# Kernel tuning notes

Measured on AMD Instinct MI355X. Metric: run time of the kernel, lower is better.

Reference implementation:

```python
import jax, jax.numpy as jnp
import numpy as np
from jax import lax

NUM_CLASSES = 9
N_BOXES = 6
LEVELS = [(32, 256), (16, 128), (8, 64), (4, 32), (2, 16), (1, 8)]
BATCH = 8


def _conv(x, w, b):
    # x: [N,C,H,W], w: [O,I,3,3] -> same-padded stride-1 conv (padding=1)
    y = lax.conv_general_dilated(x, w, window_strides=(1, 1), padding='SAME',
                                 dimension_numbers=('NCHW', 'OIHW', 'NCHW'))
    return y + b[None, :, None, None]


def _head(x, ws, bs, w_out, b_out):
    for i in range(4):
        x = jax.nn.relu(_conv(x, ws[i], bs[i]))
    return _conv(x, w_out, b_out)


def setup_inputs() -> dict:
    key = jax.random.key(0)
    ks = jax.random.split(key, 12)
    inp = {}
    for i, (h, w) in enumerate(LEVELS):
        inp[f'feat{i}'] = jax.random.normal(ks[i], (BATCH, 256, h, w), dtype=jnp.float32)
    std = 0.01  # matches _init_improved_weights: normal(0, 0.01), bias=0
    inp['reg_w'] = jax.random.normal(ks[6], (4, 256, 256, 3, 3), dtype=jnp.float32) * std
    inp['reg_b'] = jnp.zeros((4, 256), dtype=jnp.float32)
    inp['reg_w_out'] = jax.random.normal(ks[7], (N_BOXES * 4, 256, 3, 3), dtype=jnp.float32) * std
    inp['reg_b_out'] = jnp.zeros((N_BOXES * 4,), dtype=jnp.float32)
    inp['cls_w'] = jax.random.normal(ks[8], (4, 256, 256, 3, 3), dtype=jnp.float32) * std
    inp['cls_b'] = jnp.zeros((4, 256), dtype=jnp.float32)
    inp['cls_w_out'] = jax.random.normal(ks[9], (N_BOXES * NUM_CLASSES, 256, 3, 3), dtype=jnp.float32) * std
    inp['cls_b_out'] = jnp.zeros((N_BOXES * NUM_CLASSES,), dtype=jnp.float32)
    return inp


def reference(feat0, feat1, feat2, feat3, feat4, feat5,
              reg_w, reg_b, reg_w_out, reg_b_out,
              cls_w, cls_b, cls_w_out, cls_b_out):
    features = [feat0, feat1, feat2, feat3, feat4, feat5]
    locations, confidences = [], []
    for x in features:
        n = x.shape[0]
        bbox_delta = _head(x, reg_w, reg_b, reg_w_out, reg_b_out).reshape(n, 4, -1)
        bbox_conf = _head(x, cls_w, cls_b, cls_w_out, cls_b_out).reshape(n, NUM_CLASSES, -1)
        locations.append(bbox_delta)
        confidences.append(bbox_conf)
    bbox_delta = jnp.concatenate(locations, axis=2)   # [N, 4, total_anchors]
    confs = jnp.concatenate(confidences, axis=2)      # [N, num_classes, total_anchors]
    return (bbox_delta, confs)
```

## Files before the change

### kernel.cpp

```cpp
#include <hip/hip_runtime.h>
#include <hip/hip_bf16.h>


typedef float  f32x4 __attribute__((ext_vector_type(4)));
typedef int    i32x4 __attribute__((ext_vector_type(4)));
typedef int    i32x2 __attribute__((ext_vector_type(2)));
typedef __bf16 bfrag __attribute__((ext_vector_type(8)));
typedef __bf16 bf4   __attribute__((ext_vector_type(4)));

struct LevelD {
  int H, W, logW, logHW, P, HW, act_off, aoff, blk_start, pos_start;
};
struct Desc  { LevelD lv[6]; };
struct FPtrs { const float* f[6]; };

#define ACT_ELEMS  24735744
#define WREG_OFF   0
#define WCLS_OFF   2359296
#define WREGO_OFF  4718592
#define WCLSO_OFF  4773888
#define ACT0_OFF   4898304
#define ACT1_OFF   29634048
#define ACT2_OFF   54369792
#define WS_ELEMS   54369792ull
#define TOTAL_ANCH 65520
#define CLS_BASE   2096640
#define NPAD_JOBS  9264

__device__ __forceinline__ void glds16(const __bf16* g, __bf16* l) {
  __builtin_amdgcn_global_load_lds(
      (const __attribute__((address_space(1))) void*)g,
      (__attribute__((address_space(3))) void*)l, 16, 0, 0);
}

__device__ __forceinline__ int xcd_swz(int b, int nwg) {
  int xcd = b & 7;
  int q = nwg >> 3, r = nwg & 7;
  int base = (xcd < r) ? xcd * (q + 1) : r * (q + 1) + (xcd - r) * q;
  return base + (b >> 3);
}

__global__ __launch_bounds__(256) void padzero_k(__bf16* __restrict__ act, int nbuf)
{
  static const int kHh[6]   = {32, 16, 8, 4, 2, 1};
  static const int kWw[6]   = {256, 128, 64, 32, 16, 8};
  static const int kOff[6]  = {0, 17965056, 22757376, 24109056, 24526848, 24674304};
  static const int kPer[6]  = {580, 292, 148, 76, 40, 22};
  static const int kCum[7]  = {0, 4640, 6976, 8160, 8768, 9088, 9264};
  int job  = blockIdx.x * 4 + (threadIdx.x >> 6);
  int lane = threadIdx.x & 63;
  int nb = job / NPAD_JOBS;
  if (nb >= nbuf) return;
  int e8 = job - nb * NPAD_JOBS;
  int li = 0;
  #pragma unroll
  for (int i = 1; i < 6; ++i) li = (e8 >= kCum[i]) ? i : li;
  int r = e8 - kCum[li];
  int per = kPer[li];
  int n = r / per;
  int e = r - n * per;
  int H = kHh[li], W = kWw[li], Wp = W + 2;
  int y, x;
  if (e < 2 * Wp) {
    y = (e < Wp) ? 0 : (H + 1);
    x = (e < Wp) ? e : (e - Wp);
  } else {
    int e2 = e - 2 * Wp;
    x = (e2 < H) ? 0 : (W + 1);
    y = 1 + ((e2 < H) ? e2 : (e2 - H));
  }
  size_t base = (size_t)nb * ACT_ELEMS + kOff[li]
              + ((size_t)((n * (H + 2) + y) * Wp + x) << 8) + (lane << 2);
  i32x2 z = {0, 0};
  *(i32x2*)(act + base) = z;
}

__global__ __launch_bounds__(256) void prep_k(const float* __restrict__ w,
                                              __bf16* __restrict__ o, int total)
{
  for (int i = blockIdx.x * 256 + threadIdx.x; i < total; i += gridDim.x * 256) {
    int co = i / 2304;
    int r  = i - co * 2304;
    int t  = r >> 8;
    int ci = r & 255;
    o[i] = (__bf16)w[((co << 8) + ci) * 9 + t];
  }
}

__global__ __launch_bounds__(256) void convert_k(FPtrs fp, __bf16* __restrict__ act, Desc d)
{
  __shared__ __bf16 T[16 * 264];
  int b  = blockIdx.x;
  int p0 = b << 4;
  int li = 0;
  #pragma unroll
  for (int i = 1; i < 6; ++i) li = (p0 >= d.lv[i].pos_start) ? i : li;
  LevelD L = d.lv[li];
  int lp  = b * 16 - L.pos_start;
  int tid = threadIdx.x;
  int pl = tid & 15;
  int p  = lp + pl;
  int n  = p >> L.logHW;
  int y  = (p >> L.logW) & (L.H - 1);
  int x  = p & (L.W - 1);
  const float* src = fp.f[li];
  size_t base = (size_t)n * ((size_t)L.HW << 8) + (size_t)y * L.W + x;
  int c0 = tid >> 4;
  #pragma unroll
  for (int it = 0; it < 16; ++it) {
    int c = c0 + (it << 4);
    T[pl * 264 + c] = (__bf16)src[base + (size_t)c * L.HW];
  }
  __syncthreads();
  int p2 = tid >> 4;
  int cc = (tid & 15) << 4;
  int pg = lp + p2;
  int n2 = pg >> L.logHW;
  int y2 = (pg >> L.logW) & (L.H - 1);
  int x2 = pg & (L.W - 1);
  __bf16* dst = act + L.act_off +
      ((size_t)((n2 * (L.H + 2) + y2 + 1) * (L.W + 2) + x2 + 1) << 8) + cc;
  i32x4 v0 = *(const i32x4*)&T[p2 * 264 + cc];
  i32x4 v1 = *(const i32x4*)&T[p2 * 264 + cc + 8];
  *(i32x4*)dst       = v0;
  *(i32x4*)(dst + 8) = v1;
}

__global__ __launch_bounds__(512, 4)
void conv_mid_k(const __bf16* __restrict__ inb, __bf16* __restrict__ outb,
                const __bf16* __restrict__ wT, const float* __restrict__ bias,
                Desc d)
{
  __shared__ __bf16 Al[2][256 * 32];
  __shared__ __bf16 Bl[2][96 * 32];
  int b  = xcd_swz(blockIdx.x, 912);
  int li = 0;
  #pragma unroll
  for (int i = 1; i < 6; ++i) li = (b >= d.lv[i].blk_start) ? i : li;
  LevelD L = d.lv[li];
  int p0 = (b - L.blk_start) * 96;
  int tid  = threadIdx.x;
  int lane = tid & 63;
  int wv   = tid >> 6;
  int wm = wv >> 1, wn = wv & 1;
  int fr = lane & 15, fg = lane >> 4;
  int Wp = L.W + 2;

  int rsub = lane >> 2;
  int slot = lane & 3;
  int sw   = slot ^ ((rsub >> 1) & 3);

  const __bf16* gA[2];
  int ldsA[2];
  #pragma unroll
  for (int r = 0; r < 2; ++r) {
    int row = (r << 7) + (wv << 4) + rsub;
    gA[r] = wT + row * 2304 + (sw << 3);
    ldsA[r] = ((r << 7) + (wv << 4)) << 5;
  }
  const __bf16* gB;
  int ldsB;
  {
    int row = (wv << 4) + rsub;
    int p  = p0 + row;
    int pc = (p < L.P) ? p : 0;
    int n  = pc >> L.logHW;
    int y  = (pc >> L.logW) & (L.H - 1);
    int x  = pc & (L.W - 1);
    gB = inb + L.act_off + (((n * (L.H + 2) + y) * Wp + x) << 8) + (sw << 3);
    ldsB = (wv << 4) << 5;
  }

  int csw = ((fg ^ ((fr >> 1) & 3)) << 3);
  int offA[4], offB[3];
  #pragma unroll
  for (int mf = 0; mf < 4; ++mf)
    offA[mf] = (((wm << 6) + (mf << 4) + fr) << 5) + csw;
  #pragma unroll
  for (int nf = 0; nf < 3; ++nf)
    offB[nf] = ((wn * 48 + (nf << 4) + fr) << 5) + csw;

  auto stage = [&](int k, int bb) {
    int t  = k >> 3;
    int c0 = (k & 7) << 5;
    int ky = (t >= 6) ? 2 : (t >= 3 ? 1 : 0);
    int kx = t - ky * 3;
    int koffA = (t << 8) + c0;
    int koffB = ((ky * Wp + kx) << 8) + c0;
    glds16(gA[0] + koffA, &Al[bb][ldsA[0]]);
    glds16(gA[1] + koffA, &Al[bb][ldsA[1]]);
    if (wv < 6) glds16(gB + koffB, &Bl[bb][ldsB]);
  };

  f32x4 acc[4][3] = {};

  stage(0, 0);
  #pragma unroll 1
  for (int k = 0; k < 72; ++k) {
    int cur = k & 1;
    __syncthreads();
    if (k < 71) stage(k + 1, cur ^ 1);
    bfrag af[4], bfv[3];
    #pragma unroll
    for (int mf = 0; mf < 4; ++mf) af[mf]  = *(const bfrag*)&Al[cur][offA[mf]];
    #pragma unroll
    for (int nf = 0; nf < 3; ++nf) bfv[nf] = *(const bfrag*)&Bl[cur][offB[nf]];
    #pragma unroll
    for (int mf = 0; mf < 4; ++mf)
      #pragma unroll
      for (int nf = 0; nf < 3; ++nf)
        acc[mf][nf] = __builtin_amdgcn_mfma_f32_16x16x32_bf16(af[mf], bfv[nf],
                                                              acc[mf][nf], 0, 0, 0);
  }

  #pragma unroll
  for (int nf = 0; nf < 3; ++nf) {
    int pp = p0 + wn * 48 + (nf << 4) + fr;
    if (pp >= L.P) continue;
    int n2 = pp >> L.logHW;
    int y2 = (pp >> L.logW) & (L.H - 1);
    int x2 = pp & (L.W - 1);
    __bf16* ob = outb + L.act_off + (((n2 * (L.H + 2) + y2 + 1) * Wp + x2 + 1) << 8);
    #pragma unroll
    for (int mf = 0; mf < 4; ++mf) {
      int cob = (wm << 6) + (mf << 4) + (fg << 2);
      f32x4 bb = *(const f32x4*)(bias + cob);
      f32x4 v  = acc[mf][nf];
      bf4 ov;
      #pragma unroll
      for (int j = 0; j < 4; ++j) ov[j] = (__bf16)fmaxf(v[j] + bb[j], 0.0f);
      *(bf4*)(ob + cob) = ov;
    }
  }
}

__global__ __launch_bounds__(256, 3)
void conv_out_k(const __bf16* __restrict__ inb, const __bf16* __restrict__ wT,
                const float* __restrict__ biasO, float* __restrict__ dout,
                Desc d, int Cout, int isCls)
{
  __shared__ __bf16 Asm[2][64 * 32];
  __shared__ __bf16 Bsm[2][128 * 32];
  int b  = xcd_swz(blockIdx.x, 683);
  int li = 0;
  #pragma unroll
  for (int i = 1; i < 6; ++i) li = (b >= d.lv[i].blk_start) ? i : li;
  LevelD L = d.lv[li];
  int p0 = (b - L.blk_start) << 7;
  int tid  = threadIdx.x;
  int lane = tid & 63;
  int wv   = tid >> 6;
  int fr = lane & 15, fg = lane >> 4;
  int Wp = L.W + 2;
  int nmf = (Cout + 15) >> 4;

  int rsub = lane >> 2;
  int slot = lane & 3;
  int sw   = slot ^ ((rsub >> 1) & 3);

  const __bf16* gA0;
  {
    int row = (wv << 4) + rsub;
    int co  = (row < Cout) ? row : 0;
    gA0 = wT + co * 2304 + (sw << 3);
  }
  const __bf16* gB[2];
  #pragma unroll
  for (int j = 0; j < 2; ++j) {
    int row = (j << 6) + (wv << 4) + rsub;
    int p  = p0 + row;
    int pc = (p < L.P) ? p : 0;
    int n = pc >> L.logHW, y = (pc >> L.logW) & (L.H - 1), x = pc & (L.W - 1);
    gB[j] = inb + L.act_off + (((n * (L.H + 2) + y) * Wp + x) << 8) + (sw << 3);
  }
  int dW = (wv << 4) << 5;

  int csw = ((fg ^ ((fr >> 1) & 3)) << 3);
  int offA[4], offB[2];
  #pragma unroll
  for (int mf = 0; mf < 4; ++mf)
    offA[mf] = (((mf << 4) + fr) << 5) + csw;
  #pragma unroll
  for (int nf = 0; nf < 2; ++nf)
    offB[nf] = (((wv << 5) + (nf << 4) + fr) << 5) + csw;

  auto stage = [&](int k, int bb) {
    int t  = k >> 3;
    int ky = (t >= 6) ? 2 : (t >= 3 ? 1 : 0);
    int kx = t - ky * 3;
    int ka = (t << 8) + ((k & 7) << 5);
    int kb = ((ky * Wp + kx) << 8) + ((k & 7) << 5);
    glds16(gA0 + ka, &Asm[bb][dW]);
    glds16(gB[0] + kb, &Bsm[bb][dW]);
    glds16(gB[1] + kb, &Bsm[bb][2048 + dW]);
  };

  f32x4 acc[4][2] = {};

  stage(0, 0);
  #pragma unroll 1
  for (int k = 0; k < 72; ++k) {
    int cur = k & 1;
    __syncthreads();
    if (k < 71) stage(k + 1, cur ^ 1);
    bfrag af[4], bfv[2];
    #pragma unroll
    for (int mf = 0; mf < 4; ++mf)
      if (mf < nmf) af[mf] = *(const bfrag*)&Asm[cur][offA[mf]];
    #pragma unroll
    for (int nf = 0; nf < 2; ++nf)
      bfv[nf] = *(const bfrag*)&Bsm[cur][offB[nf]];
    #pragma unroll
    for (int mf = 0; mf < 4; ++mf)
      if (mf < nmf)
        #pragma unroll
        for (int nf = 0; nf < 2; ++nf)
          acc[mf][nf] = __builtin_amdgcn_mfma_f32_16x16x32_bf16(
              af[mf], bfv[nf], acc[mf][nf], 0, 0, 0);
  }

  #pragma unroll
  for (int nf = 0; nf < 2; ++nf) {
    int pp = p0 + (wv << 5) + (nf << 4) + fr;
    if (pp >= L.P) continue;
    int n2 = pp >> L.logHW;
    int y2 = (pp >> L.logW) & (L.H - 1);
    int x2 = pp & (L.W - 1);
    int sp_off = L.aoff + y2 * L.W + x2;
    #pragma unroll
    for (int mf = 0; mf < 4; ++mf) {
      if (mf < nmf) {
        #pragma unroll
        for (int j = 0; j < 4; ++j) {
          int co = (mf << 4) + (fg << 2) + j;
          if (co < Cout) {
            float val = acc[mf][nf][j] + biasO[co];
            int g   = co / 6;
            int box = co - g * 6;
            size_t idx;
            if (isCls) idx = (size_t)CLS_BASE + ((size_t)n2 * 9 + g) * TOTAL_ANCH
                             + sp_off + box * L.HW;
            else       idx = ((size_t)n2 * 4 + g) * TOTAL_ANCH + sp_off + box * L.HW;
            dout[idx] = val;
          }
        }
      }
    }
  }
}

extern "C" void kernel_launch(void* const* d_in, const int* in_sizes, int n_in,
                              void* d_out, int out_size, void* d_ws, size_t ws_size,
                              hipStream_t stream) {
  if (ws_size < WS_ELEMS * 2) return;

  static const int kH[6]      = {32, 16, 8, 4, 2, 1};
  static const int kW[6]      = {256, 128, 64, 32, 16, 8};
  static const int kLogW[6]   = {8, 7, 6, 5, 4, 3};
  static const int kLogHW[6]  = {13, 11, 9, 7, 5, 3};
  static const int kActOff[6] = {0, 17965056, 22757376, 24109056, 24526848, 24674304};
  static const int kAoff[6]   = {0, 49152, 61440, 64512, 65280, 65472};
  static const int kBlkMid[6] = {0, 683, 854, 897, 908, 911};
  static const int kBlkOut[6] = {0, 512, 640, 672, 680, 682};
  static const int kPosSt[6]  = {0, 65536, 81920, 86016, 87040, 87296};

  FPtrs fp;
  for (int i = 0; i < 6; ++i) fp.f[i] = (const float*)d_in[i];
  const float* reg_w  = (const float*)d_in[6];
  const float* reg_b  = (const float*)d_in[7];
  const float* reg_wo = (const float*)d_in[8];
  const float* reg_bo = (const float*)d_in[9];
  const float* cls_w  = (const float*)d_in[10];
  const float* cls_b  = (const float*)d_in[11];
  const float* cls_wo = (const float*)d_in[12];
  const float* cls_bo = (const float*)d_in[13];
  __bf16* ws = (__bf16*)d_ws;

  Desc dmid, dout_d;
  for (int i = 0; i < 6; ++i) {
    LevelD L;
    L.H = kH[i]; L.W = kW[i]; L.logW = kLogW[i]; L.logHW = kLogHW[i];
    L.HW = kH[i] * kW[i]; L.P = 8 * L.HW;
    L.act_off = kActOff[i]; L.aoff = kAoff[i];
    L.pos_start = kPosSt[i];
    L.blk_start = kBlkMid[i];
    dmid.lv[i] = L;
    L.blk_start = kBlkOut[i];
    dout_d.lv[i] = L;
  }

  bool use3 = ws_size >= (size_t)(ACT0_OFF + 3ull * ACT_ELEMS) * 2ull;
  int nbuf = use3 ? 3 : 2;

  padzero_k<<<(NPAD_JOBS * nbuf + 3) / 4, 256, 0, stream>>>(ws + ACT0_OFF, nbuf);

  prep_k<<<256, 256, 0, stream>>>(reg_w,  ws + WREG_OFF,  1024 * 2304);
  prep_k<<<256, 256, 0, stream>>>(cls_w,  ws + WCLS_OFF,  1024 * 2304);
  prep_k<<<64,  256, 0, stream>>>(reg_wo, ws + WREGO_OFF, 24 * 2304);
  prep_k<<<64,  256, 0, stream>>>(cls_wo, ws + WCLSO_OFF, 54 * 2304);

  if (use3) {
    convert_k<<<5460, 256, 0, stream>>>(fp, ws + ACT2_OFF, dmid);
    for (int head = 0; head < 2; ++head) {
      const __bf16* wT = ws + (head ? WCLS_OFF : WREG_OFF);
      const float*  bb = head ? cls_b : reg_b;
      conv_mid_k<<<912, 512, 0, stream>>>(ws + ACT2_OFF, ws + ACT0_OFF, wT + 0 * 589824, bb + 0,   dmid);
      conv_mid_k<<<912, 512, 0, stream>>>(ws + ACT0_OFF, ws + ACT1_OFF, wT + 1 * 589824, bb + 256, dmid);
      conv_mid_k<<<912, 512, 0, stream>>>(ws + ACT1_OFF, ws + ACT0_OFF, wT + 2 * 589824, bb + 512, dmid);
      conv_mid_k<<<912, 512, 0, stream>>>(ws + ACT0_OFF, ws + ACT1_OFF, wT + 3 * 589824, bb + 768, dmid);
      conv_out_k<<<683, 256, 0, stream>>>(ws + ACT1_OFF,
          ws + (head ? WCLSO_OFF : WREGO_OFF), head ? cls_bo : reg_bo,
          (float*)d_out, dout_d, head ? 54 : 24, head);
    }
  } else {
    for (int head = 0; head < 2; ++head) {
      convert_k<<<5460, 256, 0, stream>>>(fp, ws + ACT0_OFF, dmid);
      const __bf16* wT = ws + (head ? WCLS_OFF : WREG_OFF);
      const float*  bb = head ? cls_b : reg_b;
      conv_mid_k<<<912, 512, 0, stream>>>(ws + ACT0_OFF, ws + ACT1_OFF, wT + 0 * 589824, bb + 0,   dmid);
      conv_mid_k<<<912, 512, 0, stream>>>(ws + ACT1_OFF, ws + ACT0_OFF, wT + 1 * 589824, bb + 256, dmid);
      conv_mid_k<<<912, 512, 0, stream>>>(ws + ACT0_OFF, ws + ACT1_OFF, wT + 2 * 589824, bb + 512, dmid);
      conv_mid_k<<<912, 512, 0, stream>>>(ws + ACT1_OFF, ws + ACT0_OFF, wT + 3 * 589824, bb + 768, dmid);
      conv_out_k<<<683, 256, 0, stream>>>(ws + ACT0_OFF,
          ws + (head ? WCLSO_OFF : WREGO_OFF), head ? cls_bo : reg_bo,
          (float*)d_out, dout_d, head ? 54 : 24, head);
    }
  }
}
```

Measured before the change: 1.243 ms.

## Enlarge mid-conv tile to 256x192 with triple-buffered LDS pipeline

```diff
diff --git a/kernel.cpp b/kernel.cpp
--- a/kernel.cpp
+++ b/kernel.cpp
@@ -126,91 +126,134 @@
   *(i32x4*)(dst + 8) = v1;
 }
 
-__global__ __launch_bounds__(512, 4)
+__global__ __launch_bounds__(512, 2)
 void conv_mid_k(const __bf16* __restrict__ inb, __bf16* __restrict__ outb,
                 const __bf16* __restrict__ wT, const float* __restrict__ bias,
                 Desc d)
 {
-  __shared__ __bf16 Al[2][256 * 32];
-  __shared__ __bf16 Bl[2][96 * 32];
-  int b  = xcd_swz(blockIdx.x, 912);
+  __shared__ __bf16 Asm[3][8192];
+  __shared__ __bf16 Bsm[3][6144];
+  int b  = xcd_swz(blockIdx.x, 459);
   int li = 0;
   #pragma unroll
   for (int i = 1; i < 6; ++i) li = (b >= d.lv[i].blk_start) ? i : li;
   LevelD L = d.lv[li];
-  int p0 = (b - L.blk_start) * 96;
+  int p0 = (b - L.blk_start) * 192;
   int tid  = threadIdx.x;
   int lane = tid & 63;
   int wv   = tid >> 6;
-  int wm = wv >> 1, wn = wv & 1;
+  int wm = wv >> 2, wn = wv & 3;
   int fr = lane & 15, fg = lane >> 4;
   int Wp = L.W + 2;
 
-  int rsub = lane >> 2;
-  int slot = lane & 3;
-  int sw   = slot ^ ((rsub >> 1) & 3);
-
   const __bf16* gA[2];
   int ldsA[2];
   #pragma unroll
   for (int r = 0; r < 2; ++r) {
-    int row = (r << 7) + (wv << 4) + rsub;
+    int row = (r << 7) + (wv << 4) + (lane >> 2);
+    int sw  = (lane & 3) ^ ((row >> 1) & 3);
     gA[r] = wT + row * 2304 + (sw << 3);
     ldsA[r] = ((r << 7) + (wv << 4)) << 5;
   }
-  const __bf16* gB;
-  int ldsB;
-  {
-    int row = (wv << 4) + rsub;
+  bool bact = lane < 48;
+  const __bf16* gB[2];
+  int ldsB[2];
+  #pragma unroll
+  for (int r = 0; r < 2; ++r) {
+    int row = r * 96 + wv * 12 + (lane >> 2);
+    int sw  = (lane & 3) ^ ((row >> 1) & 3);
     int p  = p0 + row;
     int pc = (p < L.P) ? p : 0;
     int n  = pc >> L.logHW;
     int y  = (pc >> L.logW) & (L.H - 1);
     int x  = pc & (L.W - 1);
-    gB = inb + L.act_off + (((n * (L.H + 2) + y) * Wp + x) << 8) + (sw << 3);
-    ldsB = (wv << 4) << 5;
-  }
-
-  int csw = ((fg ^ ((fr >> 1) & 3)) << 3);
-  int offA[4], offB[3];
-  #pragma unroll
-  for (int mf = 0; mf < 4; ++mf)
-    offA[mf] = (((wm << 6) + (mf << 4) + fr) << 5) + csw;
-  #pragma unroll
-  for (int nf = 0; nf < 3; ++nf)
-    offB[nf] = ((wn * 48 + (nf << 4) + fr) << 5) + csw;
-
-  auto stage = [&](int k, int bb) {
-    int t  = k >> 3;
-    int c0 = (k & 7) << 5;
+    gB[r] = inb + L.act_off + (((n * (L.H + 2) + y) * Wp + x) << 8) + (sw << 3);
+    ldsB[r] = (r * 96 + wv * 12) << 5;
+  }
+
+  int offA[8], offB[3];
+  #pragma unroll
+  for (int mf = 0; mf < 8; ++mf) {
+    int row = (wm << 7) + (mf << 4) + fr;
+    offA[mf] = (row << 5) + ((fg ^ ((fr >> 1) & 3)) << 3);
+  }
+  #pragma unroll
+  for (int nf = 0; nf < 3; ++nf) {
+    int row = wn * 48 + (nf << 4) + fr;
+    offB[nf] = (row << 5) + ((fg ^ ((fr >> 1) & 3)) << 3);
+  }
+
+  auto stageA = [&](int kt, int buf) {
+    int ko = ((kt >> 3) << 8) + ((kt & 7) << 5);
+    glds16(gA[0] + ko, &Asm[buf][ldsA[0]]);
+    glds16(gA[1] + ko, &Asm[buf][ldsA[1]]);
+  };
+  auto stageB = [&](int kt, int buf) {
+    int t  = kt >> 3;
     int ky = (t >= 6) ? 2 : (t >= 3 ? 1 : 0);
     int kx = t - ky * 3;
-    int koffA = (t << 8) + c0;
-    int koffB = ((ky * Wp + kx) << 8) + c0;
-    glds16(gA[0] + koffA, &Al[bb][ldsA[0]]);
-    glds16(gA[1] + koffA, &Al[bb][ldsA[1]]);
-    if (wv < 6) glds16(gB + koffB, &Bl[bb][ldsB]);
+    int kb = ((ky * Wp + kx) << 8) + ((kt & 7) << 5);
+    if (bact) {
+      glds16(gB[0] + kb, &Bsm[buf][ldsB[0]]);
+      glds16(gB[1] + kb, &Bsm[buf][ldsB[1]]);
+    }
   };
 
-  f32x4 acc[4][3] = {};
-
-  stage(0, 0);
+  f32x4 acc[8][3] = {};
+
+  stageA(0, 0); stageB(0, 0);
+  stageA(1, 1); stageB(1, 1);
+
+  int cur = 0;
   #pragma unroll 1
-  for (int k = 0; k < 72; ++k) {
-    int cur = k & 1;
-    __syncthreads();
-    if (k < 71) stage(k + 1, cur ^ 1);
-    bfrag af[4], bfv[3];
-    #pragma unroll
-    for (int mf = 0; mf < 4; ++mf) af[mf]  = *(const bfrag*)&Al[cur][offA[mf]];
-    #pragma unroll
-    for (int nf = 0; nf < 3; ++nf) bfv[nf] = *(const bfrag*)&Bl[cur][offB[nf]];
-    #pragma unroll
-    for (int mf = 0; mf < 4; ++mf)
-      #pragma unroll
-      for (int nf = 0; nf < 3; ++nf)
-        acc[mf][nf] = __builtin_amdgcn_mfma_f32_16x16x32_bf16(af[mf], bfv[nf],
-                                                              acc[mf][nf], 0, 0, 0);
+  for (int kt = 0; kt < 72; ++kt) {
+    int sbuf = cur + 2; if (sbuf >= 3) sbuf -= 3;
+    bool st = (kt < 70);
+
+    if (kt == 71) { asm volatile("s_waitcnt vmcnt(0)" ::: "memory"); }
+    else          { asm volatile("s_waitcnt vmcnt(4)" ::: "memory"); }
+    __builtin_amdgcn_s_barrier();
+    asm volatile("" ::: "memory");
+    bfrag bf3[3], a0, a1, a2, a3;
+    #pragma unroll
+    for (int nf = 0; nf < 3; ++nf) bf3[nf] = *(const bfrag*)&Bsm[cur][offB[nf]];
+    a0 = *(const bfrag*)&Asm[cur][offA[0]];
+    a1 = *(const bfrag*)&Asm[cur][offA[1]];
+    a2 = *(const bfrag*)&Asm[cur][offA[2]];
+    a3 = *(const bfrag*)&Asm[cur][offA[3]];
+    if (st) stageA(kt + 2, sbuf);
+    asm volatile("s_waitcnt lgkmcnt(0)" ::: "memory");
+    __builtin_amdgcn_sched_barrier(0);
+    __builtin_amdgcn_s_setprio(1);
+    #pragma unroll
+    for (int nf = 0; nf < 3; ++nf) {
+      acc[0][nf] = __builtin_amdgcn_mfma_f32_16x16x32_bf16(a0, bf3[nf], acc[0][nf], 0, 0, 0);
+      acc[1][nf] = __builtin_amdgcn_mfma_f32_16x16x32_bf16(a1, bf3[nf], acc[1][nf], 0, 0, 0);
+      acc[2][nf] = __builtin_amdgcn_mfma_f32_16x16x32_bf16(a2, bf3[nf], acc[2][nf], 0, 0, 0);
+      acc[3][nf] = __builtin_amdgcn_mfma_f32_16x16x32_bf16(a3, bf3[nf], acc[3][nf], 0, 0, 0);
+    }
+    __builtin_amdgcn_s_setprio(0);
+
+    __builtin_amdgcn_s_barrier();
+    asm volatile("" ::: "memory");
+    a0 = *(const bfrag*)&Asm[cur][offA[4]];
+    a1 = *(const bfrag*)&Asm[cur][offA[5]];
+    a2 = *(const bfrag*)&Asm[cur][offA[6]];
+    a3 = *(const bfrag*)&Asm[cur][offA[7]];
+    if (st) stageB(kt + 2, sbuf);
+    asm volatile("s_waitcnt lgkmcnt(0)" ::: "memory");
+    __builtin_amdgcn_sched_barrier(0);
+    __builtin_amdgcn_s_setprio(1);
+    #pragma unroll
+    for (int nf = 0; nf < 3; ++nf) {
+      acc[4][nf] = __builtin_amdgcn_mfma_f32_16x16x32_bf16(a0, bf3[nf], acc[4][nf], 0, 0, 0);
+      acc[5][nf] = __builtin_amdgcn_mfma_f32_16x16x32_bf16(a1, bf3[nf], acc[5][nf], 0, 0, 0);
+      acc[6][nf] = __builtin_amdgcn_mfma_f32_16x16x32_bf16(a2, bf3[nf], acc[6][nf], 0, 0, 0);
+      acc[7][nf] = __builtin_amdgcn_mfma_f32_16x16x32_bf16(a3, bf3[nf], acc[7][nf], 0, 0, 0);
+    }
+    __builtin_amdgcn_s_setprio(0);
+
+    ++cur; if (cur == 3) cur = 0;
   }
 
   #pragma unroll
@@ -222,8 +265,8 @@
     int x2 = pp & (L.W - 1);
     __bf16* ob = outb + L.act_off + (((n2 * (L.H + 2) + y2 + 1) * Wp + x2 + 1) << 8);
     #pragma unroll
-    for (int mf = 0; mf < 4; ++mf) {
-      int cob = (wm << 6) + (mf << 4) + (fg << 2);
+    for (int mf = 0; mf < 8; ++mf) {
+      int cob = (wm << 7) + (mf << 4) + (fg << 2);
       f32x4 bb = *(const f32x4*)(bias + cob);
       f32x4 v  = acc[mf][nf];
       bf4 ov;
@@ -360,7 +403,7 @@
   static const int kLogHW[6]  = {13, 11, 9, 7, 5, 3};
   static const int kActOff[6] = {0, 17965056, 22757376, 24109056, 24526848, 24674304};
   static const int kAoff[6]   = {0, 49152, 61440, 64512, 65280, 65472};
-  static const int kBlkMid[6] = {0, 683, 854, 897, 908, 911};
+  static const int kBlkMid[6] = {0, 342, 428, 450, 456, 458};
   static const int kBlkOut[6] = {0, 512, 640, 672, 680, 682};
   static const int kPosSt[6]  = {0, 65536, 81920, 86016, 87040, 87296};
 
@@ -404,10 +447,10 @@
     for (int head = 0; head < 2; ++head) {
       const __bf16* wT = ws + (head ? WCLS_OFF : WREG_OFF);
       const float*  bb = head ? cls_b : reg_b;
-      conv_mid_k<<<912, 512, 0, stream>>>(ws + ACT2_OFF, ws + ACT0_OFF, wT + 0 * 589824, bb + 0,   dmid);
-      conv_mid_k<<<912, 512, 0, stream>>>(ws + ACT0_OFF, ws + ACT1_OFF, wT + 1 * 589824, bb + 256, dmid);
-      conv_mid_k<<<912, 512, 0, stream>>>(ws + ACT1_OFF, ws + ACT0_OFF, wT + 2 * 589824, bb + 512, dmid);
-      conv_mid_k<<<912, 512, 0, stream>>>(ws + ACT0_OFF, ws + ACT1_OFF, wT + 3 * 589824, bb + 768, dmid);
+      conv_mid_k<<<459, 512, 0, stream>>>(ws + ACT2_OFF, ws + ACT0_OFF, wT + 0 * 589824, bb + 0,   dmid);
+      conv_mid_k<<<459, 512, 0, stream>>>(ws + ACT0_OFF, ws + ACT1_OFF, wT + 1 * 589824, bb + 256, dmid);
+      conv_mid_k<<<459, 512, 0, stream>>>(ws + ACT1_OFF, ws + ACT0_OFF, wT + 2 * 589824, bb + 512, dmid);
+      conv_mid_k<<<459, 512, 0, stream>>>(ws + ACT0_OFF, ws + ACT1_OFF, wT + 3 * 589824, bb + 768, dmid);
       conv_out_k<<<683, 256, 0, stream>>>(ws + ACT1_OFF,
           ws + (head ? WCLSO_OFF : WREGO_OFF), head ? cls_bo : reg_bo,
           (float*)d_out, dout_d, head ? 54 : 24, head);
@@ -417,10 +460,10 @@
       convert_k<<<5460, 256, 0, stream>>>(fp, ws + ACT0_OFF, dmid);
       const __bf16* wT = ws + (head ? WCLS_OFF : WREG_OFF);
       const float*  bb = head ? cls_b : reg_b;
-      conv_mid_k<<<912, 512, 0, stream>>>(ws + ACT0_OFF, ws + ACT1_OFF, wT + 0 * 589824, bb + 0,   dmid);
-      conv_mid_k<<<912, 512, 0, stream>>>(ws + ACT1_OFF, ws + ACT0_OFF, wT + 1 * 589824, bb + 256, dmid);
-      conv_mid_k<<<912, 512, 0, stream>>>(ws + ACT0_OFF, ws + ACT1_OFF, wT + 2 * 589824, bb + 512, dmid);
-      conv_mid_k<<<912, 512, 0, stream>>>(ws + ACT1_OFF, ws + ACT0_OFF, wT + 3 * 589824, bb + 768, dmid);
+      conv_mid_k<<<459, 512, 0, stream>>>(ws + ACT0_OFF, ws + ACT1_OFF, wT + 0 * 589824, bb + 0,   dmid);
+      conv_mid_k<<<459, 512, 0, stream>>>(ws + ACT1_OFF, ws + ACT0_OFF, wT + 1 * 589824, bb + 256, dmid);
+      conv_mid_k<<<459, 512, 0, stream>>>(ws + ACT0_OFF, ws + ACT1_OFF, wT + 2 * 589824, bb + 512, dmid);
+      conv_mid_k<<<459, 512, 0, stream>>>(ws + ACT1_OFF, ws + ACT0_OFF, wT + 3 * 589824, bb + 768, dmid);
       conv_out_k<<<683, 256, 0, stream>>>(ws + ACT0_OFF,
           ws + (head ? WCLSO_OFF : WREGO_OFF), head ? cls_bo : reg_bo,
           (float*)d_out, dout_d, head ? 54 : 24, head);
```

Measured after the change: 1.208 ms. -2.8%, faster.

## Triple-buffer LDS staging in mid conv with vmcnt-based waits and setprio

Applied to the files above, without the earlier changes.

```diff
diff --git a/kernel.cpp b/kernel.cpp
--- a/kernel.cpp
+++ b/kernel.cpp
@@ -131,8 +131,8 @@
                 const __bf16* __restrict__ wT, const float* __restrict__ bias,
                 Desc d)
 {
-  __shared__ __bf16 Al[2][256 * 32];
-  __shared__ __bf16 Bl[2][96 * 32];
+  __shared__ __bf16 Asm[3][8192];
+  __shared__ __bf16 Bsm[3][3072];
   int b  = xcd_swz(blockIdx.x, 912);
   int li = 0;
   #pragma unroll
@@ -146,71 +146,88 @@
   int fr = lane & 15, fg = lane >> 4;
   int Wp = L.W + 2;
 
-  int rsub = lane >> 2;
-  int slot = lane & 3;
-  int sw   = slot ^ ((rsub >> 1) & 3);
-
   const __bf16* gA[2];
   int ldsA[2];
   #pragma unroll
   for (int r = 0; r < 2; ++r) {
-    int row = (r << 7) + (wv << 4) + rsub;
+    int row = (r << 7) + (wv << 4) + (lane >> 2);
+    int sw  = (lane & 3) ^ ((row >> 1) & 3);
     gA[r] = wT + row * 2304 + (sw << 3);
     ldsA[r] = ((r << 7) + (wv << 4)) << 5;
   }
+  bool bact = lane < 48;
   const __bf16* gB;
   int ldsB;
   {
-    int row = (wv << 4) + rsub;
+    int row = wv * 12 + (lane >> 2);
+    int sw  = (lane & 3) ^ ((row >> 1) & 3);
     int p  = p0 + row;
     int pc = (p < L.P) ? p : 0;
     int n  = pc >> L.logHW;
     int y  = (pc >> L.logW) & (L.H - 1);
     int x  = pc & (L.W - 1);
     gB = inb + L.act_off + (((n * (L.H + 2) + y) * Wp + x) << 8) + (sw << 3);
-    ldsB = (wv << 4) << 5;
-  }
-
-  int csw = ((fg ^ ((fr >> 1) & 3)) << 3);
+    ldsB = (wv * 12) << 5;
+  }
+
   int offA[4], offB[3];
   #pragma unroll
-  for (int mf = 0; mf < 4; ++mf)
-    offA[mf] = (((wm << 6) + (mf << 4) + fr) << 5) + csw;
-  #pragma unroll
-  for (int nf = 0; nf < 3; ++nf)
-    offB[nf] = ((wn * 48 + (nf << 4) + fr) << 5) + csw;
-
-  auto stage = [&](int k, int bb) {
-    int t  = k >> 3;
-    int c0 = (k & 7) << 5;
+  for (int mf = 0; mf < 4; ++mf) {
+    int row = (wm << 6) + (mf << 4) + fr;
+    offA[mf] = (row << 5) + ((fg ^ ((fr >> 1) & 3)) << 3);
+  }
+  #pragma unroll
+  for (int nf = 0; nf < 3; ++nf) {
+    int row = wn * 48 + (nf << 4) + fr;
+    offB[nf] = (row << 5) + ((fg ^ ((fr >> 1) & 3)) << 3);
+  }
+
+  auto stage = [&](int kt, int buf) {
+    int ko = ((kt >> 3) << 8) + ((kt & 7) << 5);
+    glds16(gA[0] + ko, &Asm[buf][ldsA[0]]);
+    glds16(gA[1] + ko, &Asm[buf][ldsA[1]]);
+    int t  = kt >> 3;
     int ky = (t >= 6) ? 2 : (t >= 3 ? 1 : 0);
     int kx = t - ky * 3;
-    int koffA = (t << 8) + c0;
-    int koffB = ((ky * Wp + kx) << 8) + c0;
-    glds16(gA[0] + koffA, &Al[bb][ldsA[0]]);
-    glds16(gA[1] + koffA, &Al[bb][ldsA[1]]);
-    if (wv < 6) glds16(gB + koffB, &Bl[bb][ldsB]);
+    int kb = ((ky * Wp + kx) << 8) + ((kt & 7) << 5);
+    if (bact) glds16(gB + kb, &Bsm[buf][ldsB]);
   };
 
   f32x4 acc[4][3] = {};
 
   stage(0, 0);
+  stage(1, 1);
+
+  int cur = 0;
   #pragma unroll 1
-  for (int k = 0; k < 72; ++k) {
-    int cur = k & 1;
-    __syncthreads();
-    if (k < 71) stage(k + 1, cur ^ 1);
-    bfrag af[4], bfv[3];
-    #pragma unroll
-    for (int mf = 0; mf < 4; ++mf) af[mf]  = *(const bfrag*)&Al[cur][offA[mf]];
-    #pragma unroll
-    for (int nf = 0; nf < 3; ++nf) bfv[nf] = *(const bfrag*)&Bl[cur][offB[nf]];
-    #pragma unroll
-    for (int mf = 0; mf < 4; ++mf)
-      #pragma unroll
-      for (int nf = 0; nf < 3; ++nf)
-        acc[mf][nf] = __builtin_amdgcn_mfma_f32_16x16x32_bf16(af[mf], bfv[nf],
-                                                              acc[mf][nf], 0, 0, 0);
+  for (int kt = 0; kt < 72; ++kt) {
+    int sbuf = cur + 2; if (sbuf >= 3) sbuf -= 3;
+    if (kt == 71) { asm volatile("s_waitcnt vmcnt(0)" ::: "memory"); }
+    else          { asm volatile("s_waitcnt vmcnt(3)" ::: "memory"); }
+    __builtin_amdgcn_s_barrier();
+    asm volatile("" ::: "memory");
+
+    bfrag bf3[3], a0, a1, a2, a3;
+    #pragma unroll
+    for (int nf = 0; nf < 3; ++nf) bf3[nf] = *(const bfrag*)&Bsm[cur][offB[nf]];
+    a0 = *(const bfrag*)&Asm[cur][offA[0]];
+    a1 = *(const bfrag*)&Asm[cur][offA[1]];
+    a2 = *(const bfrag*)&Asm[cur][offA[2]];
+    a3 = *(const bfrag*)&Asm[cur][offA[3]];
+    if (kt < 70) stage(kt + 2, sbuf);
+    asm volatile("s_waitcnt lgkmcnt(0)" ::: "memory");
+    __builtin_amdgcn_sched_barrier(0);
+    __builtin_amdgcn_s_setprio(1);
+    #pragma unroll
+    for (int nf = 0; nf < 3; ++nf) {
+      acc[0][nf] = __builtin_amdgcn_mfma_f32_16x16x32_bf16(a0, bf3[nf], acc[0][nf], 0, 0, 0);
+      acc[1][nf] = __builtin_amdgcn_mfma_f32_16x16x32_bf16(a1, bf3[nf], acc[1][nf], 0, 0, 0);
+      acc[2][nf] = __builtin_amdgcn_mfma_f32_16x16x32_bf16(a2, bf3[nf], acc[2][nf], 0, 0, 0);
+      acc[3][nf] = __builtin_amdgcn_mfma_f32_16x16x32_bf16(a3, bf3[nf], acc[3][nf], 0, 0, 0);
+    }
+    __builtin_amdgcn_s_setprio(0);
+
+    ++cur; if (cur == 3) cur = 0;
   }
 
   #pragma unroll
```

Measured after the change: 1.190 ms (median of 3 runs). 4.3% less time.
